# Performance work log

Measured on AMD Instinct MI355X. Metric: run time of the kernel, lower is better.

Reference implementation:

```python
import math
import jax, jax.numpy as jnp
import numpy as np

N_TOKENS = 2048
HIDDEN = 2880
HEAD_DIM = 64
N_HEADS = 64          # total attention heads
N_KV = 8              # key/value heads
Q_MULT = N_HEADS // N_KV
SLIDING_WINDOW = 128  # layer_idx=0 (even) -> window active
ROPE_BASE = 150000.0
INIT_CTX = 4096.0
ROPE_SCALE = 32.0
NTK_ALPHA = 1.0
NTK_BETA = 32.0
QKV_DIM = HEAD_DIM * (N_HEADS + 2 * N_KV)  # 5120
EPS = 1e-5
NEG = -1e30


def _cos_sin(n_tokens):
    # YaRN-scaled rotary tables (scaling_factor > 1 branch)
    freq = ROPE_BASE ** (jnp.arange(0, HEAD_DIM, 2, dtype=jnp.float32) / HEAD_DIM)
    concentration = 0.1 * jnp.log(jnp.float32(ROPE_SCALE)) + 1.0
    d_half = HEAD_DIM / 2
    log_base = jnp.log(jnp.float32(ROPE_BASE))
    low = d_half * jnp.log(jnp.float32(INIT_CTX / (NTK_BETA * 2 * np.pi))) / log_base
    high = d_half * jnp.log(jnp.float32(INIT_CTX / (NTK_ALPHA * 2 * np.pi))) / log_base
    interpolation = 1.0 / (ROPE_SCALE * freq)
    extrapolation = 1.0 / freq
    ramp = (jnp.arange(d_half, dtype=jnp.float32) - low) / (high - low)
    mask = 1.0 - jnp.clip(ramp, 0.0, 1.0)
    inv_freq = interpolation * (1.0 - mask) + extrapolation * mask
    t = jnp.arange(n_tokens, dtype=jnp.float32)
    freqs = t[:, None] * inv_freq[None, :]          # [n, head_dim//2]
    return jnp.cos(freqs) * concentration, jnp.sin(freqs) * concentration


def _apply_rotary(x, cos, sin):
    # x: [n, heads, head_dim]; cos/sin: [n, head_dim//2]
    cos = cos[:, None, :].astype(x.dtype)
    sin = sin[:, None, :].astype(x.dtype)
    x1, x2 = jnp.split(x, 2, axis=-1)
    return jnp.concatenate((x1 * cos - x2 * sin, x2 * cos + x1 * sin), axis=-1)


def _rmsnorm(x, scale):
    t = x.astype(jnp.float32)
    rms = jnp.sqrt(jnp.mean(t * t, axis=-1, keepdims=True) + EPS)
    return (t / rms * scale).astype(x.dtype)


def _sdpa(q, k, v, sinks):
    # q: [n, h_kv, q_mult, d]; k, v: [n, h_kv, d]; sinks: [n_heads]
    n = q.shape[0]
    sm_scale = 1.0 / math.sqrt(HEAD_DIM)
    q32, k32, v32 = q.astype(jnp.float32), k.astype(jnp.float32), v.astype(jnp.float32)
    qk = jnp.einsum('qhmd,khd->hmqk', q32, k32) * jnp.float32(sm_scale)
    i = jnp.arange(n)
    # causal AND within sliding window: q - window < k <= q
    allowed = (i[None, :] <= i[:, None]) & (i[None, :] > i[:, None] - SLIDING_WINDOW)
    qk = qk + jnp.where(allowed, jnp.float32(0.0), jnp.float32(NEG))[None, None, :, :]
    s = sinks.astype(jnp.float32).reshape(N_KV, Q_MULT, 1, 1)
    s = jnp.broadcast_to(s, (N_KV, Q_MULT, n, 1))
    w = jax.nn.softmax(jnp.concatenate([qk, s], axis=-1), axis=-1)[..., :-1]
    attn = jnp.einsum('hmqk,khd->qhmd', w, v32)
    return attn.astype(q.dtype).reshape(n, -1)  # [n, n_heads*head_dim]


def setup_inputs() -> dict:
    key = jax.random.key(0)
    ks = jax.random.split(key, 5)
    s = 0.02
    return {
        'x': jax.random.normal(ks[0], (N_TOKENS, HIDDEN), jnp.float32),
        'norm_scale': jnp.ones((HIDDEN,), jnp.float32),
        'w_qkv': jax.random.normal(ks[1], (HIDDEN, QKV_DIM), jnp.float32) * s,
        'b_qkv': jnp.zeros((QKV_DIM,), jnp.float32),
        'sinks': jax.random.normal(ks[2], (N_HEADS,), jnp.float32),
        'w_out': jax.random.normal(ks[3], (N_HEADS * HEAD_DIM, HIDDEN), jnp.float32) * s,
        'b_out': jnp.zeros((HIDDEN,), jnp.float32),
    }


def reference(x, norm_scale, w_qkv, b_qkv, sinks, w_out, b_out):
    n = x.shape[0]
    t = _rmsnorm(x, norm_scale)
    qkv = t @ w_qkv + b_qkv                                   # [n, qkv_dim]
    q_end = N_HEADS * HEAD_DIM
    k_end = q_end + N_KV * HEAD_DIM
    q = qkv[:, :q_end].reshape(n, N_KV, Q_MULT, HEAD_DIM)
    k = qkv[:, q_end:k_end].reshape(n, N_KV, HEAD_DIM)
    v = qkv[:, k_end:].reshape(n, N_KV, HEAD_DIM)
    cos, sin = _cos_sin(n)
    q = _apply_rotary(q.reshape(n, -1, HEAD_DIM), cos, sin).reshape(n, N_KV, Q_MULT, HEAD_DIM)
    k = _apply_rotary(k, cos, sin)
    attn = _sdpa(q, k, v, sinks)                              # [n, n_heads*head_dim]
    return x + (attn @ w_out + b_out)
```

## Files before the change

### kernel.cpp

```cpp
#include <hip/hip_runtime.h>
#include <hip/hip_bf16.h>
#include <math.h>

#define N_TOK 2048
#define HIDDEN 2880
#define QKV_DIM 5120
#define LOG2E 1.44269504088896340736f

typedef __attribute__((ext_vector_type(8))) short short8;
typedef __attribute__((ext_vector_type(4))) float f32x4;
typedef __attribute__((ext_vector_type(16))) float f32x16;

__device__ __forceinline__ float bf2f(unsigned short u) {
  union { unsigned int i; float f; } c; c.i = ((unsigned int)u) << 16; return c.f;
}
__device__ __forceinline__ unsigned short f2bf(float f) {
  union { float f; unsigned int i; } c; c.f = f;
  unsigned int i = c.i;
  return (unsigned short)((i + 0x7FFFu + ((i >> 16) & 1u)) >> 16);
}
__device__ __forceinline__ void gload16(const void* g, void* l) {
  __builtin_amdgcn_global_load_lds((const __attribute__((address_space(1))) void*)g,
                                   (__attribute__((address_space(3))) void*)l, 16, 0, 0);
}

__global__ __launch_bounds__(256) void prep_kernel(
    const float* __restrict__ w_qkv, unsigned short* __restrict__ wqkvT,
    const float* __restrict__ w_out, unsigned short* __restrict__ woutT,
    const float* __restrict__ x, const float* __restrict__ scale,
    unsigned short* __restrict__ t_bf)
{
  __shared__ float tile[64][65];
  int b = blockIdx.x;
  const int t = threadIdx.x;
  if (b >= 6480) {
    int row = b - 6480;
    const float* xr = x + (size_t)row * HIDDEN;
    float ss = 0.f;
    for (int i = t; i < HIDDEN / 4; i += 256) {
      float4 v = ((const float4*)xr)[i];
      ss += v.x * v.x + v.y * v.y + v.z * v.z + v.w * v.w;
    }
#pragma unroll
    for (int off = 32; off; off >>= 1) ss += __shfl_down(ss, off, 64);
    __shared__ float red[4];
    if ((t & 63) == 0) red[t >> 6] = ss;
    __syncthreads();
    float total = red[0] + red[1] + red[2] + red[3];
    float rinv = rsqrtf(total / (float)HIDDEN + 1e-5f);
    for (int i = t; i < HIDDEN / 4; i += 256) {
      float4 v = ((const float4*)xr)[i];
      float4 s4 = ((const float4*)scale)[i];
      union { unsigned short u[4]; uint2 p; } pk;
      pk.u[0] = f2bf(v.x * rinv * s4.x);
      pk.u[1] = f2bf(v.y * rinv * s4.y);
      pk.u[2] = f2bf(v.z * rinv * s4.z);
      pk.u[3] = f2bf(v.w * rinv * s4.w);
      *(uint2*)&t_bf[(size_t)row * HIDDEN + i * 4] = pk.p;
    }
    return;
  }
  const float* in; unsigned short* out; int R, C, bx, by;
  if (b < 3600) { in = w_qkv; out = wqkvT; R = 2880; C = 5120; bx = b % 80; by = b / 80; }
  else { b -= 3600; in = w_out; out = woutT; R = 4096; C = 2880; bx = b % 45; by = b / 45; }
  const int r0 = by * 64, c0 = bx * 64;
  const int c4 = t & 15, rr = t >> 4;
#pragma unroll
  for (int p = 0; p < 4; ++p) {
    int row = rr + p * 16;
    float4 v = *(const float4*)&in[(size_t)(r0 + row) * C + c0 + c4 * 4];
    tile[row][c4 * 4 + 0] = v.x; tile[row][c4 * 4 + 1] = v.y;
    tile[row][c4 * 4 + 2] = v.z; tile[row][c4 * 4 + 3] = v.w;
  }
  __syncthreads();
  const int rc = t & 7;
#pragma unroll
  for (int it = 0; it < 2; ++it) {
    int cc = (t >> 3) + it * 32;
    unsigned short tmp[8];
#pragma unroll
    for (int i = 0; i < 8; ++i) tmp[i] = f2bf(tile[rc * 8 + i][cc]);
    *(uint4*)&out[(size_t)(c0 + cc) * R + r0 + rc * 8] = *(uint4*)tmp;
  }
}

template <int NF, int EPI>
__global__ __launch_bounds__(512, 2) void gemm8(
    const unsigned short* __restrict__ A,
    const unsigned short* __restrict__ Bt,
    const float* __restrict__ bias,
    const float* __restrict__ resid,
    void* __restrict__ Cout,
    int K, int Ncols)
{
  constexpr int BUFSZ = 16384 + NF * 8192;
  constexpr int NCH = 2 + NF;
  constexpr int HALF = NCH / 2;
  __shared__ char smem_[2 * BUFSZ];
  const int tid = threadIdx.x;
  const int lane = tid & 63;
  const int w = tid >> 6;
  const int fr = lane & 15, fq = lane >> 4;
  const int wr = w >> 2, wc = w & 3;

  const int nwg = gridDim.x;
  const int cpx = nwg >> 3;
  const int wg = (blockIdx.x & 7) * cpx + (blockIdx.x >> 3);
  const int by = wg & 15, bx = wg >> 4;
  const int row0 = by * 128, col0 = bx * (NF * 64);

  const unsigned short* gsrc[NCH];
  int ldsoff[NCH];
#pragma unroll
  for (int c = 0; c < NCH; ++c) {
    int g = tid + 512 * c;
    if (g < 1024) {
      int kk = g >> 9, rr = (g >> 2) & 127, u = g & 3;
      gsrc[c] = A + (size_t)(row0 + rr) * K + kk * 32 + ((u ^ ((rr >> 1) & 3)) * 8);
      ldsoff[c] = kk * 8192 + rr * 64 + u * 16;
    } else {
      int g2 = g - 1024;
      int kk = g2 / (NF * 256);
      int rm = g2 - kk * (NF * 256);
      int rr = rm >> 2, u = rm & 3;
      gsrc[c] = Bt + (size_t)(col0 + rr) * K + kk * 32 + ((u ^ ((rr >> 1) & 3)) * 8);
      ldsoff[c] = 16384 + kk * (NF * 4096) + rr * 64 + u * 16;
    }
  }
  const int urd = (fq ^ ((fr >> 1) & 3)) * 16;
  const int aoffb = (wr * 64 + fr) * 64 + urd;
  const int boffb = 16384 + (wc * NF * 16 + fr) * 64 + urd;

  f32x4 acc[4][NF];
#pragma unroll
  for (int mf = 0; mf < 4; ++mf)
#pragma unroll
    for (int nf = 0; nf < NF; ++nf) acc[mf][nf] = (f32x4)0.f;

  const int NT = K >> 6;

#define ISSUE(c) gload16(gsrc[c] + ktn, smem_ + nbufo + ldsoff[c])
#define RD_A(mf, kk) (*(const short8*)(smem_ + bufo + (kk)*8192 + (mf)*1024 + aoffb))
#define RD_B(nf, kk) (*(const short8*)(smem_ + bufo + (kk)*(NF*4096) + (nf)*1024 + boffb))

  {
    const int ktn = 0, nbufo = 0;
#pragma unroll
    for (int c = 0; c < NCH; ++c) gload16(gsrc[c] + ktn, smem_ + nbufo + ldsoff[c]);
  }

  for (int t = 0; t < NT; ++t) {
    const int bufo = (t & 1) * BUFSZ;
    const int nbufo = bufo ^ BUFSZ;
    const int ktn = (t + 1) * 64;
    const bool pref = (t + 1) < NT;

    asm volatile("s_waitcnt vmcnt(0)" ::: "memory");
    __builtin_amdgcn_s_barrier();

    if (pref) {
#pragma unroll
      for (int c = 0; c < HALF; ++c) ISSUE(c);
    }

    short8 afr[4], bfr[NF];
#pragma unroll
    for (int nf = 0; nf < NF; ++nf) bfr[nf] = RD_B(nf, 0);
#pragma unroll
    for (int mf = 0; mf < 4; ++mf) afr[mf] = RD_A(mf, 0);
    __builtin_amdgcn_s_setprio(1);
#pragma unroll
    for (int mf = 0; mf < 4; ++mf)
#pragma unroll
      for (int nf = 0; nf < NF; ++nf)
        acc[mf][nf] = __builtin_amdgcn_mfma_f32_16x16x32_bf16(afr[mf], bfr[nf], acc[mf][nf], 0, 0, 0);
    __builtin_amdgcn_s_setprio(0);

    if (pref) {
#pragma unroll
      for (int c = HALF; c < NCH; ++c) ISSUE(c);
    }

#pragma unroll
    for (int nf = 0; nf < NF; ++nf) bfr[nf] = RD_B(nf, 1);
#pragma unroll
    for (int mf = 0; mf < 4; ++mf) afr[mf] = RD_A(mf, 1);
    __builtin_amdgcn_s_setprio(1);
#pragma unroll
    for (int mf = 0; mf < 4; ++mf)
#pragma unroll
      for (int nf = 0; nf < NF; ++nf)
        acc[mf][nf] = __builtin_amdgcn_mfma_f32_16x16x32_bf16(afr[mf], bfr[nf], acc[mf][nf], 0, 0, 0);
    __builtin_amdgcn_s_setprio(0);
  }
#undef ISSUE
#undef RD_A
#undef RD_B

#pragma unroll
  for (int mf = 0; mf < 4; ++mf) {
#pragma unroll
    for (int nf = 0; nf < NF; ++nf) {
      const int colb = col0 + wc * NF * 16 + nf * 16 + fr;
      const int rowb = row0 + wr * 64 + mf * 16 + fq * 4;
      const float bs = bias[colb];
      if (EPI == 1) {
#pragma unroll
        for (int j = 0; j < 4; ++j)
          ((unsigned short*)Cout)[(size_t)(rowb + j) * Ncols + colb] =
              f2bf(acc[mf][nf][j] + bs);
      } else {
#pragma unroll
        for (int j = 0; j < 4; ++j) {
          const size_t idx = (size_t)(rowb + j) * Ncols + colb;
          ((float*)Cout)[idx] = acc[mf][nf][j] + bs + resid[idx];
        }
      }
    }
  }
}

__global__ __launch_bounds__(256) void rope_kernel(unsigned short* __restrict__ qkv)
{
  __shared__ float cs[32], sn[32];
  const int token = blockIdx.x;
  const int t = threadIdx.x;
  if (t < 32) {
    const float log_base = 11.9183905731f;
    float fj = (float)t;
    float extrap = expf(-log_base * fj * 0.03125f);
    float interp = extrap * 0.03125f;
    const float low  = 32.f * logf(4096.f / (32.f * 6.283185307179586f)) / log_base;
    const float high = 32.f * logf(4096.f / 6.283185307179586f) / log_base;
    float ramp = (fj - low) / (high - low);
    float maskv = 1.f - fminf(fmaxf(ramp, 0.f), 1.f);
    float inv_freq = interp * (1.f - maskv) + extrap * maskv;
    float ang = (float)token * inv_freq;
    const float conc = 1.3465735903f;
    float s, c;
    sincosf(ang, &s, &c);
    cs[t] = c * conc; sn[t] = s * conc;
  }
  __syncthreads();
  for (int p = t; p < 72 * 32; p += 256) {
    int h = p >> 5, j = p & 31;
    size_t base = (size_t)token * QKV_DIM + h * 64 + j;
    float c = cs[j], s = sn[j];
    float x1 = bf2f(qkv[base]), x2 = bf2f(qkv[base + 32]);
    qkv[base]      = f2bf(x1 * c - x2 * s);
    qkv[base + 32] = f2bf(x2 * c + x1 * s);
  }
}

__global__ __launch_bounds__(512) void attn_kernel(
    const unsigned short* __restrict__ qkv, const float* __restrict__ sinks,
    unsigned short* __restrict__ attn)
{
  __shared__ unsigned short Ks[160 * 64];
  __shared__ unsigned short Vt[64 * 192];
  const int tid  = threadIdx.x;
  const int lane = tid & 63;
  const int w    = tid >> 6;
  const int qb = blockIdx.x, kvh = blockIdx.y;
  const int q0 = qb * 32;
  const int kb = q0 - 128;
  const int h  = lane >> 5;
  const int ql = lane & 31;

  for (int it = w; it < 20; it += 8) {
    int r = it * 8 + (lane >> 3);
    int s = lane & 7;
    int j = kb + r; if (j < 0) j = 0;
    const unsigned short* src =
        qkv + (size_t)j * QKV_DIM + 4096 + kvh * 64 + ((s ^ (r & 7)) * 8);
    gload16(src, &Ks[r * 64 + s * 8]);
  }
  for (int c = tid; c < 2560; c += 512) {
    int jl = c >> 4;
    int d4 = (c & 15) * 4;
    int j = kb + jl; if (j < 0) j = 0;
    ushort4 v4 = *(const ushort4*)&qkv[(size_t)j * QKV_DIM + 4608 + kvh * 64 + d4];
    const unsigned short* pv = (const unsigned short*)&v4;
#pragma unroll
    for (int t = 0; t < 4; ++t) {
      int d = d4 + t;
      int slot = (jl >> 3) ^ (d & 7);
      Vt[d * 192 + slot * 8 + (jl & 7)] = pv[t];
    }
  }
  const int head = kvh * 8 + w;
  const int i_q = q0 + ql;
  short8 qf[4];
  {
    const unsigned short* qp = qkv + (size_t)i_q * QKV_DIM + head * 64 + h * 8;
#pragma unroll
    for (int ks = 0; ks < 4; ++ks) qf[ks] = *(const short8*)(qp + ks * 16);
  }
  __syncthreads();

  const float SC = 0.125f * LOG2E;
  f32x16 oacc0 = (f32x16)(0.f), oacc1 = (f32x16)(0.f);
  float m = -1e30f, l = 0.f;

  const int tstart = qb < 4 ? 4 - qb : 0;
  for (int tt = tstart; tt < 5; ++tt) {
    const int j0 = kb + tt * 32;
    f32x16 sacc = (f32x16)(0.f);
    const int kr = tt * 32 + ql;
#pragma unroll
    for (int ks = 0; ks < 4; ++ks) {
      short8 kf = *(const short8*)&Ks[kr * 64 + (((ks * 2 + h) ^ (kr & 7)) * 8)];
      sacc = __builtin_amdgcn_mfma_f32_32x32x16_bf16(kf, qf[ks], sacc, 0, 0, 0);
    }
    float sc16[16];
    float mt = -INFINITY;
#pragma unroll
    for (int e = 0; e < 16; ++e) {
      int kk = (e & 3) + 8 * (e >> 2) + 4 * h;
      int j = j0 + kk;
      float s2 = sacc[e] * SC;
      bool valid = (j <= i_q) && (j > i_q - 128);
      s2 = valid ? s2 : -INFINITY;
      sc16[e] = s2;
      mt = fmaxf(mt, s2);
    }
    mt = fmaxf(mt, __shfl_xor(mt, 32));
    float mnew = fmaxf(m, mt);
    float r = exp2f(m - mnew);
    l *= r;
    oacc0 *= r;
    oacc1 *= r;
    m = mnew;
    unsigned int wpk[8];
    float ls = 0.f;
#pragma unroll
    for (int e2 = 0; e2 < 8; ++e2) {
      float plo = exp2f(sc16[2 * e2]     - m);
      float phi = exp2f(sc16[2 * e2 + 1] - m);
      ls += plo + phi;
      asm("v_cvt_pk_bf16_f32 %0, %1, %2" : "=v"(wpk[e2]) : "v"(plo), "v"(phi));
    }
    l += ls;
#pragma unroll
    for (int m16 = 0; m16 < 2; ++m16) {
      int go = 2 * m16 + h;
      int gs = 2 * m16 + 1 - h;
      unsigned int x0 = (unsigned int)__shfl_xor((int)wpk[2 * gs],     32);
      unsigned int x1 = (unsigned int)__shfl_xor((int)wpk[2 * gs + 1], 32);
      union { unsigned int u[4]; short8 s; } bu;
      bu.u[0] = h ? x0 : wpk[2 * go];
      bu.u[1] = h ? x1 : wpk[2 * go + 1];
      bu.u[2] = h ? wpk[2 * go]     : x0;
      bu.u[3] = h ? wpk[2 * go + 1] : x1;
      short8 bfrag = bu.s;
#pragma unroll
      for (int dt = 0; dt < 2; ++dt) {
        int d = dt * 32 + ql;
        int slot = (tt * 4 + m16 * 2 + h) ^ (d & 7);
        short8 vf = *(const short8*)&Vt[d * 192 + slot * 8];
        if (dt == 0)
          oacc0 = __builtin_amdgcn_mfma_f32_32x32x16_bf16(vf, bfrag, oacc0, 0, 0, 0);
        else
          oacc1 = __builtin_amdgcn_mfma_f32_32x32x16_bf16(vf, bfrag, oacc1, 0, 0, 0);
      }
    }
  }
  float lt = l + __shfl_xor(l, 32);
  lt += exp2f(sinks[head] * LOG2E - m);
  float inv = 1.f / lt;
  unsigned short* op = attn + (size_t)i_q * 4096 + head * 64;
#pragma unroll
  for (int dt = 0; dt < 2; ++dt) {
#pragma unroll
    for (int g = 0; g < 4; ++g) {
      float f0, f1, f2, f3;
      if (dt == 0) {
        f0 = oacc0[4 * g]; f1 = oacc0[4 * g + 1]; f2 = oacc0[4 * g + 2]; f3 = oacc0[4 * g + 3];
      } else {
        f0 = oacc1[4 * g]; f1 = oacc1[4 * g + 1]; f2 = oacc1[4 * g + 2]; f3 = oacc1[4 * g + 3];
      }
      unsigned int u0, u1;
      asm("v_cvt_pk_bf16_f32 %0, %1, %2" : "=v"(u0) : "v"(f0 * inv), "v"(f1 * inv));
      asm("v_cvt_pk_bf16_f32 %0, %1, %2" : "=v"(u1) : "v"(f2 * inv), "v"(f3 * inv));
      int d = dt * 32 + 8 * g + 4 * h;
      uint2 pr; pr.x = u0; pr.y = u1;
      *(uint2*)(op + d) = pr;
    }
  }
}

extern "C" void kernel_launch(void* const* d_in, const int* in_sizes, int n_in,
                              void* d_out, int out_size, void* d_ws, size_t ws_size,
                              hipStream_t stream)
{
  const float* x      = (const float*)d_in[0];
  const float* nscale = (const float*)d_in[1];
  const float* w_qkv  = (const float*)d_in[2];
  const float* b_qkv  = (const float*)d_in[3];
  const float* sinks  = (const float*)d_in[4];
  const float* w_out  = (const float*)d_in[5];
  const float* b_out  = (const float*)d_in[6];

  char* ws = (char*)d_ws;
  unsigned short* t_bf  = (unsigned short*)(ws);
  unsigned short* wqkvT = (unsigned short*)(ws + 11796480);
  unsigned short* qkv   = (unsigned short*)(ws + 41287680);
  unsigned short* attn  = (unsigned short*)(ws + 62259200);
  unsigned short* woutT = (unsigned short*)(ws + 79036416);

  prep_kernel<<<8528, 256, 0, stream>>>(w_qkv, wqkvT, w_out, woutT, x, nscale, t_bf);
  gemm8<5, 1><<<256, 512, 0, stream>>>(t_bf, wqkvT, b_qkv, nullptr, (void*)qkv, 2880, 5120);
  rope_kernel<<<N_TOK, 256, 0, stream>>>(qkv);
  attn_kernel<<<dim3(64, 8), 512, 0, stream>>>(qkv, sinks, attn);
  gemm8<3, 2><<<240, 512, 0, stream>>>(attn, woutT, b_out, x, d_out, 4096, 2880);
}
```

Before: 183.3 us.

## Fuse RoPE into attention loads using precomputed cos/sin tables

Removes the standalone rope kernel, which read and rewrote the Q and K columns of the qkv buffer. The YaRN cos/sin tables are now computed by extra blocks of the prep kernel, and the attention kernel applies the rotation to K as it stages it into shared memory and to Q in registers. The K staging changes from async global-to-LDS loads to register loads plus explicit LDS stores. K rows are re-rotated by every query block that overlaps them (about 5x redundancy), in exchange for saving one launch and a full pass over qkv.

Result: faster. 178.5 us (-2.6%).

```diff
diff --git a/kernel.cpp b/kernel.cpp
--- a/kernel.cpp
+++ b/kernel.cpp
@@ -28,11 +28,36 @@
     const float* __restrict__ w_qkv, unsigned short* __restrict__ wqkvT,
     const float* __restrict__ w_out, unsigned short* __restrict__ woutT,
     const float* __restrict__ x, const float* __restrict__ scale,
-    unsigned short* __restrict__ t_bf)
+    unsigned short* __restrict__ t_bf,
+    float* __restrict__ cstab, float* __restrict__ sntab)
 {
   __shared__ float tile[64][65];
   int b = blockIdx.x;
   const int t = threadIdx.x;
+  if (b >= 8528) {
+    const float log_base = 11.9183905731f;
+    const float low  = 32.f * logf(4096.f / (32.f * 6.283185307179586f)) / log_base;
+    const float high = 32.f * logf(4096.f / 6.283185307179586f) / log_base;
+    const float conc = 1.3465735903f;
+    int e0 = (b - 8528) * 1024 + t * 4;
+#pragma unroll
+    for (int k = 0; k < 4; ++k) {
+      int entry = e0 + k;
+      int token = entry >> 5, d = entry & 31;
+      float fj = (float)d;
+      float extrap = expf(-log_base * fj * 0.03125f);
+      float interp = extrap * 0.03125f;
+      float ramp = (fj - low) / (high - low);
+      float maskv = 1.f - fminf(fmaxf(ramp, 0.f), 1.f);
+      float inv_freq = interp * (1.f - maskv) + extrap * maskv;
+      float ang = (float)token * inv_freq;
+      float s, c;
+      sincosf(ang, &s, &c);
+      cstab[entry] = c * conc;
+      sntab[entry] = s * conc;
+    }
+    return;
+  }
   if (b >= 6480) {
     int row = b - 6480;
     const float* xr = x + (size_t)row * HIDDEN;
@@ -220,40 +245,9 @@
   }
 }
 
-__global__ __launch_bounds__(256) void rope_kernel(unsigned short* __restrict__ qkv)
-{
-  __shared__ float cs[32], sn[32];
-  const int token = blockIdx.x;
-  const int t = threadIdx.x;
-  if (t < 32) {
-    const float log_base = 11.9183905731f;
-    float fj = (float)t;
-    float extrap = expf(-log_base * fj * 0.03125f);
-    float interp = extrap * 0.03125f;
-    const float low  = 32.f * logf(4096.f / (32.f * 6.283185307179586f)) / log_base;
-    const float high = 32.f * logf(4096.f / 6.283185307179586f) / log_base;
-    float ramp = (fj - low) / (high - low);
-    float maskv = 1.f - fminf(fmaxf(ramp, 0.f), 1.f);
-    float inv_freq = interp * (1.f - maskv) + extrap * maskv;
-    float ang = (float)token * inv_freq;
-    const float conc = 1.3465735903f;
-    float s, c;
-    sincosf(ang, &s, &c);
-    cs[t] = c * conc; sn[t] = s * conc;
-  }
-  __syncthreads();
-  for (int p = t; p < 72 * 32; p += 256) {
-    int h = p >> 5, j = p & 31;
-    size_t base = (size_t)token * QKV_DIM + h * 64 + j;
-    float c = cs[j], s = sn[j];
-    float x1 = bf2f(qkv[base]), x2 = bf2f(qkv[base + 32]);
-    qkv[base]      = f2bf(x1 * c - x2 * s);
-    qkv[base + 32] = f2bf(x2 * c + x1 * s);
-  }
-}
-
 __global__ __launch_bounds__(512) void attn_kernel(
     const unsigned short* __restrict__ qkv, const float* __restrict__ sinks,
+    const float* __restrict__ cstab, const float* __restrict__ sntab,
     unsigned short* __restrict__ attn)
 {
   __shared__ unsigned short Ks[160 * 64];
@@ -267,13 +261,27 @@
   const int h  = lane >> 5;
   const int ql = lane & 31;
 
-  for (int it = w; it < 20; it += 8) {
-    int r = it * 8 + (lane >> 3);
-    int s = lane & 7;
+  for (int task = tid; task < 640; task += 512) {
+    int r = task >> 2, p = task & 3;
     int j = kb + r; if (j < 0) j = 0;
-    const unsigned short* src =
-        qkv + (size_t)j * QKV_DIM + 4096 + kvh * 64 + ((s ^ (r & 7)) * 8);
-    gload16(src, &Ks[r * 64 + s * 8]);
+    const unsigned short* kp = qkv + (size_t)j * QKV_DIM + 4096 + kvh * 64 + p * 8;
+    short8 klo = *(const short8*)kp;
+    short8 khi = *(const short8*)(kp + 32);
+    float cv[8], sv[8];
+    *(float4*)&cv[0] = *(const float4*)&cstab[j * 32 + p * 8];
+    *(float4*)&cv[4] = *(const float4*)&cstab[j * 32 + p * 8 + 4];
+    *(float4*)&sv[0] = *(const float4*)&sntab[j * 32 + p * 8];
+    *(float4*)&sv[4] = *(const float4*)&sntab[j * 32 + p * 8 + 4];
+    unsigned short nlo[8], nhi[8];
+#pragma unroll
+    for (int e = 0; e < 8; ++e) {
+      float lo = bf2f(((const unsigned short*)&klo)[e]);
+      float hi = bf2f(((const unsigned short*)&khi)[e]);
+      nlo[e] = f2bf(lo * cv[e] - hi * sv[e]);
+      nhi[e] = f2bf(hi * cv[e] + lo * sv[e]);
+    }
+    *(short8*)&Ks[r * 64 + ((p ^ (r & 7)) * 8)]       = *(short8*)nlo;
+    *(short8*)&Ks[r * 64 + (((p + 4) ^ (r & 7)) * 8)] = *(short8*)nhi;
   }
   for (int c = tid; c < 2560; c += 512) {
     int jl = c >> 4;
@@ -295,6 +303,25 @@
     const unsigned short* qp = qkv + (size_t)i_q * QKV_DIM + head * 64 + h * 8;
 #pragma unroll
     for (int ks = 0; ks < 4; ++ks) qf[ks] = *(const short8*)(qp + ks * 16);
+#pragma unroll
+    for (int p = 0; p < 2; ++p) {
+      float cv[8], sv[8];
+      int o = i_q * 32 + p * 16 + h * 8;
+      *(float4*)&cv[0] = *(const float4*)&cstab[o];
+      *(float4*)&cv[4] = *(const float4*)&cstab[o + 4];
+      *(float4*)&sv[0] = *(const float4*)&sntab[o];
+      *(float4*)&sv[4] = *(const float4*)&sntab[o + 4];
+      unsigned short nlo[8], nhi[8];
+#pragma unroll
+      for (int e = 0; e < 8; ++e) {
+        float lo = bf2f(((const unsigned short*)&qf[p])[e]);
+        float hi = bf2f(((const unsigned short*)&qf[p + 2])[e]);
+        nlo[e] = f2bf(lo * cv[e] - hi * sv[e]);
+        nhi[e] = f2bf(hi * cv[e] + lo * sv[e]);
+      }
+      qf[p]     = *(short8*)nlo;
+      qf[p + 2] = *(short8*)nhi;
+    }
   }
   __syncthreads();
 
@@ -407,10 +434,12 @@
   unsigned short* qkv   = (unsigned short*)(ws + 41287680);
   unsigned short* attn  = (unsigned short*)(ws + 62259200);
   unsigned short* woutT = (unsigned short*)(ws + 79036416);
-
-  prep_kernel<<<8528, 256, 0, stream>>>(w_qkv, wqkvT, w_out, woutT, x, nscale, t_bf);
+  float* cstab          = (float*)(ws + 102629376);
+  float* sntab          = (float*)(ws + 102891520);
+
+  prep_kernel<<<8592, 256, 0, stream>>>(w_qkv, wqkvT, w_out, woutT, x, nscale, t_bf,
+                                        cstab, sntab);
   gemm8<5, 1><<<256, 512, 0, stream>>>(t_bf, wqkvT, b_qkv, nullptr, (void*)qkv, 2880, 5120);
-  rope_kernel<<<N_TOK, 256, 0, stream>>>(qkv);
-  attn_kernel<<<dim3(64, 8), 512, 0, stream>>>(qkv, sinks, attn);
+  attn_kernel<<<dim3(64, 8), 512, 0, stream>>>(qkv, sinks, cstab, sntab, attn);
   gemm8<3, 2><<<240, 512, 0, stream>>>(attn, woutT, b_out, x, d_out, 4096, 2880);
 }
```
